# Kernel optimization log

Hardware: AMD Instinct MI355X
Metric: run time of the kernel (lower is better)

## Reference

```python
import jax, jax.numpy as jnp
import numpy as np

N_NODES = 10000
DIM = 512
HEADS = 8
HEAD_DIM = DIM // HEADS  # 64
TOPK = 6
EPS = 1e-5
SLOPE = 0.01  # torch LeakyReLU default


def _layernorm(x, w, b):
    mu = x.mean(axis=-1, keepdims=True)
    var = ((x - mu) ** 2).mean(axis=-1, keepdims=True)
    return (x - mu) / jnp.sqrt(var + EPS) * w + b


def setup_inputs() -> dict:
    key = jax.random.key(0)
    ks = jax.random.split(key, 8)

    def w(k, shape):
        return jax.random.normal(k, shape, dtype=jnp.float32) * 0.02

    return {
        "x": jax.random.normal(ks[0], (1, N_NODES, DIM), dtype=jnp.float32),
        "fc1_w": w(ks[1], (DIM, DIM)), "fc1_b": jnp.zeros((DIM,), jnp.float32),
        "wh_w": w(ks[2], (DIM, DIM)), "wh_b": jnp.zeros((DIM,), jnp.float32),
        "wt_w": w(ks[3], (DIM, DIM)), "wt_b": jnp.zeros((DIM,), jnp.float32),
        "q_w": w(ks[4], (DIM, DIM)), "q_b": jnp.zeros((DIM,), jnp.float32),
        "kv_w": w(ks[5], (2 * DIM, DIM)), "kv_b": jnp.zeros((2 * DIM,), jnp.float32),
        "lin_w": w(ks[6], (DIM, DIM)), "lin_b": jnp.zeros((DIM,), jnp.float32),
        "norm_w": jnp.ones((DIM,), jnp.float32),
        "norm_b": jnp.zeros((DIM,), jnp.float32),
    }


def reference(x, fc1_w, fc1_b, wh_w, wh_b, wt_w, wt_b, q_w, q_b,
              kv_w, kv_b, lin_w, lin_b, norm_w, norm_b):
    # x: [1, N, DIM]
    n = x.shape[1]
    scale = HEAD_DIM ** -0.5

    x_input = x
    h = jax.nn.leaky_relu(x @ fc1_w.T + fc1_b, SLOPE)
    h = (h + h.mean(axis=1, keepdims=True)) * 0.5

    e_h = h @ wh_w.T + wh_b            # [1, N, DIM]
    e_t = h @ wt_w.T + wt_b            # [1, N, DIM]

    # dense graph-construction scores + per-row top-k neighbors
    logits = (e_h * scale) @ jnp.swapaxes(e_t, -2, -1)   # [1, N, N]
    _, topk_idx = jax.lax.top_k(logits, TOPK)            # [1, N, TOPK]

    # prototype node = most frequent tail index (torch unique+counts+argsort, top=1)
    counts = jnp.bincount(topk_idx.reshape(-1), length=n)
    top_node = jnp.argmax(counts)

    ins_top = jnp.take(x_input, top_node[None], axis=1)  # [1, 1, DIM]
    q_feat = jnp.take(h, top_node[None], axis=1)[0, 0]   # [DIM]

    # gather k=TOPK neighbor tail embeddings per node
    nb = e_t[0][topk_idx[0]]                              # [N, TOPK, DIM]

    q_heads = (q_feat @ q_w.T + q_b).reshape(HEADS, HEAD_DIM) * scale
    kv = (nb @ kv_w.T + kv_b).reshape(n, TOPK, 2, HEADS, HEAD_DIM)
    k_, v_ = kv[:, :, 0], kv[:, :, 1]                     # [N, TOPK, H, HD]

    attn = jnp.einsum('hd,nehd->nhe', q_heads, k_)        # [N, H, TOPK]
    attn = jax.nn.softmax(attn, axis=-1)
    out = jnp.einsum('nhe,nehd->nhd', attn, v_).reshape(n, DIM)

    e_nh = _layernorm(out, norm_w, norm_b)[None]          # [1, N, DIM]

    s = _layernorm(e_h + e_nh, norm_w, norm_b)
    s = jax.nn.leaky_relu(s @ lin_w.T + lin_b, SLOPE)     # dropout = identity (eval)
    embedding = s + x_input
    return embedding, ins_top
```

## Files before the change

kernel.cpp:

```cpp
#include <hip/hip_runtime.h>
#include <hip/hip_bf16.h>
#include <math.h>

#define N_NODES 10000
#define DIM 512
#define TOPK 6
#define NCHUNK 10
#define CHUNK 1024
#define NL 4
#define NCK 8
#define NC2 16
#define SLOPE 0.01
#define LN_EPS 1e-5f
#define NB_COL 320

typedef short bf16x8 __attribute__((ext_vector_type(8)));
typedef float f32x4 __attribute__((ext_vector_type(4)));
typedef double f64x4 __attribute__((ext_vector_type(4)));

__device__ __forceinline__ unsigned pack_key(float v, int idx)
{
    unsigned b = __float_as_uint(v);
    unsigned m = b ^ ((unsigned)((int)b >> 31) | 0x80000000u);
    return (m & 0xFFFFC000u) | (16383u - (unsigned)idx);
}

template <int D>
__device__ __forceinline__ void insert_u(unsigned (&k)[D], unsigned nk)
{
    if (nk > k[D - 1]) {
        k[D - 1] = nk;
#pragma unroll
        for (int s = D - 1; s > 0; s--) {
            unsigned hi = max(k[s], k[s - 1]);
            unsigned lo = min(k[s], k[s - 1]);
            k[s - 1] = hi; k[s] = lo;
        }
    }
}

__device__ __forceinline__ void gload16(const void* g, void* l)
{
    __builtin_amdgcn_global_load_lds(
        (const __attribute__((address_space(1))) void*)g,
        (__attribute__((address_space(3))) void*)l, 16, 0, 0);
}

__global__ __launch_bounds__(256) void colsum_part64(
    const double* __restrict__ h, double* __restrict__ part, int n, int nb)
{
    int b = blockIdx.x;
    int rows_per = (n + nb - 1) / nb;
    int r0 = b * rows_per, r1 = min(n, r0 + rows_per);
    int t = threadIdx.x;
    double s0 = 0.0, s1 = 0.0;
    for (int i = r0; i < r1; i++) {
        s0 += h[(size_t)i * DIM + t];
        s1 += h[(size_t)i * DIM + t + 256];
    }
    part[b * DIM + t] = s0;
    part[b * DIM + t + 256] = s1;
}

__global__ void colmean64(const double* __restrict__ part, double* __restrict__ mean,
                          int nb, int n)
{
    int j = blockIdx.x * blockDim.x + threadIdx.x;
    if (j < DIM) {
        double s = 0.0;
        for (int b = 0; b < nb; b++) s += part[b * DIM + j];
        mean[j] = s / (double)n;
    }
}

__global__ void cast_wb(const float* __restrict__ in1, short* __restrict__ o1, int n1,
                        const float* __restrict__ in2, short* __restrict__ o2)
{
    int i = (blockIdx.x * blockDim.x + threadIdx.x) * 4;
    const float* in = (i < n1) ? in1 + i : in2 + (i - n1);
    short* o = (i < n1) ? o1 + i : o2 + (i - n1);
    float4 f = *(const float4*)in;
    __hip_bfloat16 b0 = __float2bfloat16(f.x), b1 = __float2bfloat16(f.y);
    __hip_bfloat16 b2 = __float2bfloat16(f.z), b3 = __float2bfloat16(f.w);
    *(short4*)o = make_short4(*(short*)&b0, *(short*)&b1, *(short*)&b2, *(short*)&b3);
}

__global__ __launch_bounds__(256, 4) void gemm_fc1(
    const float* __restrict__ X, const float* __restrict__ W,
    const float* __restrict__ bias, double* __restrict__ C, int n)
{
    const int K = DIM, M = DIM;
    const int id = blockIdx.x;
    const int c = id & 7, kk2 = id >> 3;
    const int y = kk2 & 3, mm = kk2 >> 2;
    const int bx = c + 8 * mm;
    if (bx >= (n + 63) / 64) return;

    __shared__ double As[64][18];
    __shared__ double Bs[128][18];
    const int t = threadIdx.x, lane = t & 63, wid = t >> 6;
    const int lx = lane & 15, q = lane >> 4;
    const int wr = (wid >> 1) * 32, wc = (wid & 1) * 64;
    const int i0 = bx * 64, j0 = y * 128;

    f64x4 acc[2][4];
#pragma unroll
    for (int a = 0; a < 2; a++)
#pragma unroll
        for (int b = 0; b < 4; b++) acc[a][b] = (f64x4)0.0;

    const int arow = t >> 2, askq = (t & 3) * 4;
    int gi = i0 + arow; if (gi >= n) gi = n - 1;
    const float* af32 = X + (size_t)gi * K + askq;
    const int brow = t >> 1, bskq = (t & 1) * 8;
    const float* wrow = W + (size_t)(j0 + brow) * K + bskq;

    float4 wv0 = *(const float4*)(wrow);
    float4 wv1 = *(const float4*)(wrow + 4);
    float4 av = *(const float4*)(af32);

    for (int k0 = 0; k0 < K; k0 += 16) {
        __syncthreads();
        As[arow][askq]     = (double)av.x; As[arow][askq + 1] = (double)av.y;
        As[arow][askq + 2] = (double)av.z; As[arow][askq + 3] = (double)av.w;
        Bs[brow][bskq]     = (double)wv0.x; Bs[brow][bskq + 1] = (double)wv0.y;
        Bs[brow][bskq + 2] = (double)wv0.z; Bs[brow][bskq + 3] = (double)wv0.w;
        Bs[brow][bskq + 4] = (double)wv1.x; Bs[brow][bskq + 5] = (double)wv1.y;
        Bs[brow][bskq + 6] = (double)wv1.z; Bs[brow][bskq + 7] = (double)wv1.w;
        if (k0 + 16 < K) {
            wv0 = *(const float4*)(wrow + k0 + 16);
            wv1 = *(const float4*)(wrow + k0 + 20);
            av  = *(const float4*)(af32 + k0 + 16);
        }
        __syncthreads();

#pragma unroll
        for (int ks = 0; ks < 4; ks++) {
            double a0 = As[wr + lx][ks * 4 + q];
            double a1 = As[wr + 16 + lx][ks * 4 + q];
#pragma unroll
            for (int cf = 0; cf < 4; cf++) {
                double b = Bs[wc + cf * 16 + lx][ks * 4 + q];
                acc[0][cf] = __builtin_amdgcn_mfma_f64_16x16x4f64(a0, b, acc[0][cf], 0, 0, 0);
                acc[1][cf] = __builtin_amdgcn_mfma_f64_16x16x4f64(a1, b, acc[1][cf], 0, 0, 0);
            }
        }
    }

#pragma unroll
    for (int rf = 0; rf < 2; rf++)
#pragma unroll
        for (int cf = 0; cf < 4; cf++)
#pragma unroll
            for (int reg = 0; reg < 4; reg++) {
                int gi2 = i0 + wr + rf * 16 + q * 4 + reg;
                int gj2 = j0 + wc + cf * 16 + lx;
                if (gi2 < n) {
                    double v = acc[rf][cf][reg] + (double)bias[gj2];
                    v = (v >= 0.0) ? v : v * SLOPE;
                    C[(size_t)gi2 * M + gj2] = v;
                }
            }
}

__global__ __launch_bounds__(256, 4) void gemm_ehet(
    const double* __restrict__ H, const float* __restrict__ whw,
    const float* __restrict__ whb, const float* __restrict__ wtw,
    const float* __restrict__ wtb, const double* __restrict__ mn,
    double* __restrict__ ehd, float* __restrict__ ehf, short* __restrict__ ehb2,
    double* __restrict__ etd, short* __restrict__ etb2, int n)
{
    const int K = DIM, M = DIM;
    const int id = blockIdx.x;
    const int c = id & 7, kk2 = id >> 3;
    const int y = kk2 & 7, mm = kk2 >> 3;
    const int bx = c + 8 * mm;
    if (bx >= (n + 63) / 64) return;
    const bool isH = (y < 4);
    const float* W    = isH ? whw : wtw;
    const float* bias = isH ? whb : wtb;
    double* C  = isH ? ehd : etd;
    short*  ob = isH ? ehb2 : etb2;

    __shared__ double As[64][18];
    __shared__ double Bs[128][18];
    const int t = threadIdx.x, lane = t & 63, wid = t >> 6;
    const int lx = lane & 15, q = lane >> 4;
    const int wr = (wid >> 1) * 32, wc = (wid & 1) * 64;
    const int i0 = bx * 64, j0 = (y & 3) * 128;

    f64x4 acc[2][4];
#pragma unroll
    for (int a = 0; a < 2; a++)
#pragma unroll
        for (int b = 0; b < 4; b++) acc[a][b] = (f64x4)0.0;

    const int arow = t >> 2, askq = (t & 3) * 4;
    int gi = i0 + arow; if (gi >= n) gi = n - 1;
    const double* af64 = H + (size_t)gi * K + askq;
    const int brow = t >> 1, bskq = (t & 1) * 8;
    const float* wrow = W + (size_t)(j0 + brow) * K + bskq;

    float4 wv0 = *(const float4*)(wrow);
    float4 wv1 = *(const float4*)(wrow + 4);
    double2 a0v = *(const double2*)(af64);
    double2 a1v = *(const double2*)(af64 + 2);

    for (int k0 = 0; k0 < K; k0 += 16) {
        __syncthreads();
        double2 mv0 = *(const double2*)(mn + k0 + askq);
        double2 mv1 = *(const double2*)(mn + k0 + askq + 2);
        As[arow][askq]     = (a0v.x + mv0.x) * 0.5; As[arow][askq + 1] = (a0v.y + mv0.y) * 0.5;
        As[arow][askq + 2] = (a1v.x + mv1.x) * 0.5; As[arow][askq + 3] = (a1v.y + mv1.y) * 0.5;
        Bs[brow][bskq]     = (double)wv0.x; Bs[brow][bskq + 1] = (double)wv0.y;
        Bs[brow][bskq + 2] = (double)wv0.z; Bs[brow][bskq + 3] = (double)wv0.w;
        Bs[brow][bskq + 4] = (double)wv1.x; Bs[brow][bskq + 5] = (double)wv1.y;
        Bs[brow][bskq + 6] = (double)wv1.z; Bs[brow][bskq + 7] = (double)wv1.w;
        if (k0 + 16 < K) {
            wv0 = *(const float4*)(wrow + k0 + 16);
            wv1 = *(const float4*)(wrow + k0 + 20);
            a0v = *(const double2*)(af64 + k0 + 16);
            a1v = *(const double2*)(af64 + k0 + 18);
        }
        __syncthreads();

#pragma unroll
        for (int ks = 0; ks < 4; ks++) {
            double a0 = As[wr + lx][ks * 4 + q];
            double a1 = As[wr + 16 + lx][ks * 4 + q];
#pragma unroll
            for (int cf = 0; cf < 4; cf++) {
                double b = Bs[wc + cf * 16 + lx][ks * 4 + q];
                acc[0][cf] = __builtin_amdgcn_mfma_f64_16x16x4f64(a0, b, acc[0][cf], 0, 0, 0);
                acc[1][cf] = __builtin_amdgcn_mfma_f64_16x16x4f64(a1, b, acc[1][cf], 0, 0, 0);
            }
        }
    }

#pragma unroll
    for (int rf = 0; rf < 2; rf++)
#pragma unroll
        for (int cf = 0; cf < 4; cf++)
#pragma unroll
            for (int reg = 0; reg < 4; reg++) {
                int gi2 = i0 + wr + rf * 16 + q * 4 + reg;
                int gj2 = j0 + wc + cf * 16 + lx;
                if (gi2 < n) {
                    double v = acc[rf][cf][reg] + (double)bias[gj2];
                    size_t idx = (size_t)gi2 * M + gj2;
                    C[idx] = v;
                    float f = (float)v;
                    if (isH) ehf[idx] = f;
                    __hip_bfloat16 bb = __float2bfloat16(f);
                    ob[idx] = *reinterpret_cast<short*>(&bb);
                }
            }
}

__global__ __launch_bounds__(256, 3) void logits_topk_mfma(
    const short* __restrict__ eh, const short* __restrict__ et,
    unsigned* __restrict__ pk, int n)
{
    __shared__ short As[2][4096];
    __shared__ short Bs[2][4096];
    const int t = threadIdx.x;
    const int lane = t & 63, wid = t >> 6;
    const int lx = lane & 15, q = lane >> 4;

    int id = blockIdx.x, bx, chunk;
    if (id < 632) { chunk = id & 7; bx = id >> 3; }
    else { int r = id - 632; chunk = 8 + (r & 1); bx = r >> 1; }
    const int i0 = bx * 128;
    const int wbase = wid * 32;

    const int jlo = chunk * CHUNK;
    const int jhi = min(n, jlo + CHUNK);
    const int nj = (jhi - jlo + 127) >> 7;
    const int np = nj * 16;

    const int sslot = (t & 3) ^ ((t >> 3) & 3);
    const short* aP[2];
    const short* bP[2];
#pragma unroll
    for (int is = 0; is < 2; is++) {
        int row = is * 64 + (t >> 2);
        int ra = i0 + row; if (ra >= n) ra = n - 1;
        aP[is] = eh + (size_t)ra * DIM + sslot * 8;
    }
    const int slotq = (q ^ ((lx >> 1) & 3)) * 8;
    const int aOff = (wbase + lx) * 32 + slotq;
    const int bOff = lx * 32 + slotq;

    unsigned keys[8][NL];
#pragma unroll
    for (int r = 0; r < 8; r++)
#pragma unroll
        for (int s = 0; s < NL; s++) keys[r][s] = 0u;

    f32x4 acc[2][8];
#pragma unroll
    for (int rf = 0; rf < 2; rf++)
#pragma unroll
        for (int cf = 0; cf < 8; cf++) acc[rf][cf] = (f32x4)0.f;

    auto STAGE = [&](int buf, int ph) {
        int kk = ph & 15;
        if (kk == 0) {
            int j0 = jlo + (ph >> 4) * 128;
#pragma unroll
            for (int is = 0; is < 2; is++) {
                int row = is * 64 + (t >> 2);
                int rb = j0 + row; if (rb >= n) rb = n - 1;
                bP[is] = et + (size_t)rb * DIM + sslot * 8;
            }
        }
        int ko = kk * 32;
#pragma unroll
        for (int is = 0; is < 2; is++) {
            gload16(aP[is] + ko, &As[buf][is * 2048 + wid * 512]);
            gload16(bP[is] + ko, &Bs[buf][is * 2048 + wid * 512]);
        }
    };

    STAGE(0, 0);
    for (int p = 0; p < np; ++p) {
        __builtin_amdgcn_sched_barrier(0);
        __builtin_amdgcn_s_barrier();
        __builtin_amdgcn_sched_barrier(0);
        if (p + 1 < np) {
            STAGE((p + 1) & 1, p + 1);
            asm volatile("s_waitcnt vmcnt(4)" ::: "memory");
        } else {
            asm volatile("s_waitcnt vmcnt(0)" ::: "memory");
        }
        __builtin_amdgcn_sched_barrier(0);
        __builtin_amdgcn_s_barrier();
        __builtin_amdgcn_sched_barrier(0);

        const short* Ab = As[p & 1];
        const short* Bb = Bs[p & 1];
        bf16x8 a0 = *(const bf16x8*)(Ab + aOff);
        bf16x8 a1 = *(const bf16x8*)(Ab + aOff + 512);
#pragma unroll
        for (int cf = 0; cf < 8; cf++) {
            bf16x8 bw = *(const bf16x8*)(Bb + bOff + cf * 512);
            acc[0][cf] = __builtin_amdgcn_mfma_f32_16x16x32_bf16(
                a0, bw, acc[0][cf], 0, 0, 0);
            acc[1][cf] = __builtin_amdgcn_mfma_f32_16x16x32_bf16(
                a1, bw, acc[1][cf], 0, 0, 0);
        }

        if ((p & 15) == 15) {
            int j0 = jlo + (p >> 4) * 128;
#pragma unroll
            for (int rf = 0; rf < 2; rf++)
#pragma unroll
                for (int cf = 0; cf < 8; cf++) {
                    int gj = j0 + cf * 16 + lx;
                    if (gj < n) {
#pragma unroll
                        for (int reg = 0; reg < 4; reg++)
                            insert_u<NL>(keys[rf * 4 + reg],
                                         pack_key(acc[rf][cf][reg], gj));
                    }
                    acc[rf][cf] = (f32x4)0.f;
                }
        }
    }

#pragma unroll
    for (int rr = 0; rr < 8; rr++) {
        unsigned mk[NCK];
#pragma unroll
        for (int s = 0; s < NL; s++) mk[s] = keys[rr][s];
#pragma unroll
        for (int s = NL; s < NCK; s++) mk[s] = 0u;
        for (int m = 1; m < 16; m <<= 1) {
            unsigned sv[NCK];
#pragma unroll
            for (int s = 0; s < NCK; s++) sv[s] = mk[s];
#pragma unroll
            for (int s = 0; s < NCK; s++) {
                unsigned ov = (unsigned)__shfl_xor((int)sv[s], m);
                insert_u<NCK>(mk, ov);
            }
        }
        if (lx == 0) {
            int rf = rr >> 2, reg = rr & 3;
            int grow = i0 + wbase + rf * 16 + q * 4 + reg;
            if (grow < n) {
#pragma unroll
                for (int s = 0; s < NCK; s++)
                    pk[((size_t)chunk * N_NODES + grow) * NCK + s] = mk[s];
            }
        }
    }
}

template <int POST, int NY, int LY>
__global__ __launch_bounds__(256, 3) void mfma_gemm_bf16(
    const short* __restrict__ A, const short* __restrict__ W,
    const float* __restrict__ bias, const float* __restrict__ res,
    float* __restrict__ C, int n, int M)
{
    const int id = blockIdx.x;
    const int c = id & 7, kk2 = id >> 3;
    const int y = kk2 & (NY - 1), mm = kk2 >> LY;
    const int bxx = c + 8 * mm;
    if (bxx >= (n + 127) / 128) return;

    __shared__ short As[2][8192];
    __shared__ short Bs[2][8192];
    const int t = threadIdx.x;
    const int lane = t & 63, wid = t >> 6;
    const int lx = lane & 15, q = lane >> 4;
    const int lx7 = lane & 7;
    const int i0 = bxx * 128;
    const int j0 = y * 128;
    const int wbase = wid * 32;
    const int srl = lane >> 3;
    const int swz = (lane & 7) ^ srl;

    const short* aP[4];
    const short* bP[4];
#pragma unroll
    for (int is = 0; is < 4; is++) {
        int ra = i0 + is * 32 + wid * 8 + srl; if (ra >= n) ra = n - 1;
        aP[is] = A + (size_t)ra * DIM + swz * 8;
        int rb = j0 + is * 32 + wid * 8 + srl;
        bP[is] = W + (size_t)rb * DIM + swz * 8;
    }
    int aIdx[2], bIdx[2];
#pragma unroll
    for (int ks = 0; ks < 2; ks++) {
        int kap = (ks * 4 + q) ^ lx7;
        aIdx[ks] = (wbase + lx) * 64 + kap * 8;
        bIdx[ks] = lx * 64 + kap * 8;
    }

    f32x4 acc[2][8];
#pragma unroll
    for (int rf = 0; rf < 2; rf++)
#pragma unroll
        for (int cf = 0; cf < 8; cf++) acc[rf][cf] = (f32x4)0.f;

    auto STAGE = [&](int buf, int kk) {
        int ko = kk * 64;
        short* ab = &As[buf][wid * 512];
        short* bb = &Bs[buf][wid * 512];
#pragma unroll
        for (int is = 0; is < 4; is++) {
            gload16(aP[is] + ko, ab + is * 2048);
            gload16(bP[is] + ko, bb + is * 2048);
        }
    };

    STAGE(0, 0);
    for (int p = 0; p < 8; ++p) {
        __builtin_amdgcn_sched_barrier(0);
        __builtin_amdgcn_s_barrier();
        __builtin_amdgcn_sched_barrier(0);
        if (p + 1 < 8) {
            STAGE((p + 1) & 1, p + 1);
            asm volatile("s_waitcnt vmcnt(8)" ::: "memory");
        } else {
            asm volatile("s_waitcnt vmcnt(0)" ::: "memory");
        }
        __builtin_amdgcn_sched_barrier(0);
        __builtin_amdgcn_s_barrier();
        __builtin_amdgcn_sched_barrier(0);

        const short* Ab = As[p & 1];
        const short* Bb = Bs[p & 1];
#pragma unroll
        for (int ks = 0; ks < 2; ks++) {
            bf16x8 a0 = *(const bf16x8*)(Ab + aIdx[ks]);
            bf16x8 a1 = *(const bf16x8*)(Ab + aIdx[ks] + 1024);
#pragma unroll
            for (int cf = 0; cf < 8; cf++) {
                bf16x8 bw = *(const bf16x8*)(Bb + bIdx[ks] + cf * 1024);
                acc[0][cf] = __builtin_amdgcn_mfma_f32_16x16x32_bf16(
                    a0, bw, acc[0][cf], 0, 0, 0);
                acc[1][cf] = __builtin_amdgcn_mfma_f32_16x16x32_bf16(
                    a1, bw, acc[1][cf], 0, 0, 0);
            }
        }
    }

#pragma unroll
    for (int rf = 0; rf < 2; rf++)
#pragma unroll
        for (int cf = 0; cf < 8; cf++)
#pragma unroll
            for (int reg = 0; reg < 4; reg++) {
                int gi = i0 + wbase + rf * 16 + q * 4 + reg;
                int gj = j0 + cf * 16 + lx;
                if (gi < n) {
                    float v = acc[rf][cf][reg] + bias[gj];
                    if (POST >= 1) v = (v >= 0.f) ? v : v * SLOPE;
                    if (POST == 2) v += res[(size_t)gi * M + gj];
                    C[(size_t)gi * M + gj] = v;
                }
            }
}

__global__ void merge_chunks16(const unsigned* __restrict__ pk,
                               int* __restrict__ cand, int n)
{
    int row = blockIdx.x * blockDim.x + threadIdx.x;
    if (row >= n) return;
    unsigned bk[NC2];
#pragma unroll
    for (int s = 0; s < NC2; s++) bk[s] = 0u;
    for (int c = 0; c < NCHUNK; c++) {
#pragma unroll
        for (int s = 0; s < NCK; s++)
            insert_u<NC2>(bk, pk[((size_t)c * n + row) * NCK + s]);
    }
#pragma unroll
    for (int s = 0; s < NC2; s++)
        cand[row * NC2 + s] = 16383 - (int)(bk[s] & 16383u);
}

__global__ __launch_bounds__(256) void refine16(
    const double* __restrict__ ehd, const double* __restrict__ etd,
    const int* __restrict__ cand, int* __restrict__ tki,
    int* __restrict__ counts, int n)
{
    int row = blockIdx.x * 4 + (threadIdx.x >> 6);
    if (row >= n) return;
    int lane = threadIdx.x & 63;
    int c = lane >> 2, sub = lane & 3;
    int j = cand[row * NC2 + c];
    const double* er = ehd + (size_t)row * DIM;
    const double* tr = etd + (size_t)j * DIM;
    double s = 0.0;
#pragma unroll 8
    for (int k = sub; k < DIM; k += 4) s += er[k] * tr[k];
    s += __shfl_down(s, 2);
    s += __shfl_down(s, 1);
    double mine = __shfl(s, lane & ~3);
    int rank = 0;
#pragma unroll
    for (int m = 0; m < NC2; m++) {
        double vm = __shfl(s, m * 4);
        int jm = __shfl(j, m * 4);
        bool better = (vm > mine) || (vm == mine && jm < j);
        rank += better ? 1 : 0;
    }
    if (sub == 0 && rank < TOPK) {
        tki[row * TOPK + rank] = j;
        atomicAdd(&counts[j], 1);
    }
}

__global__ __launch_bounds__(1024) void argmax_kernel(
    const int* __restrict__ counts, int n, const float* __restrict__ x,
    int* __restrict__ topn, float* __restrict__ out_ins)
{
    __shared__ unsigned long long red[1024];
    int t = threadIdx.x;
    unsigned long long best = 0;
    for (int j = t; j < n; j += 1024) {
        unsigned long long key =
            ((unsigned long long)(unsigned)counts[j] << 32) | (unsigned)(n - 1 - j);
        if (key > best) best = key;
    }
    red[t] = best;
    __syncthreads();
    for (int s = 512; s > 0; s >>= 1) {
        if (t < s && red[t + s] > red[t]) red[t] = red[t + s];
        __syncthreads();
    }
    int tn = n - 1 - (int)(red[0] & 0xffffffffu);
    if (t == 0) *topn = tn;
    if (t < DIM) out_ins[t] = x[(size_t)tn * DIM + t];
}

__global__ __launch_bounds__(512) void qheads_kernel(
    const double* __restrict__ h2d, const double* __restrict__ mn,
    const int* __restrict__ topn, const float* __restrict__ qw,
    const float* __restrict__ qb, float* __restrict__ qh)
{
    __shared__ float qf[DIM];
    int t = threadIdx.x;
    int tn = *topn;
    qf[t] = (float)((h2d[(size_t)tn * DIM + t] + mn[t]) * 0.5);
    __syncthreads();
    int w = t >> 6, lane = t & 63;
    int jrow = blockIdx.x * 8 + w;
    float s = 0.f;
    for (int k = lane; k < DIM; k += 64) s += qf[k] * qw[(size_t)jrow * DIM + k];
#pragma unroll
    for (int m = 32; m > 0; m >>= 1) s += __shfl_down(s, m);
    if (lane == 0) qh[jrow] = (s + qb[jrow]) * 0.125f;
}

__global__ __launch_bounds__(512) void scores_kernel(
    const float* __restrict__ E, const float* __restrict__ qh, float* __restrict__ sc)
{
    int i = blockIdx.x;
    int t = threadIdx.x, w = t >> 6, lane = t & 63;
    float v = qh[t] * E[(size_t)i * 1024 + t];
#pragma unroll
    for (int m = 32; m > 0; m >>= 1) v += __shfl_down(v, m);
    if (lane == 0) sc[i * 8 + w] = v;
}

__global__ __launch_bounds__(512) void attn_ln_kernel(
    const float* __restrict__ E, const float* __restrict__ sc,
    const int* __restrict__ tki, const float* __restrict__ eh,
    const float* __restrict__ nw, const float* __restrict__ nbias,
    short* __restrict__ sprb, int n)
{
    __shared__ int nb[TOPK];
    __shared__ float red[16];
    __shared__ float stats[2];
    const int i = blockIdx.x;
    const int t = threadIdx.x;
    const int h = t >> 6, lane = t & 63;
    if (t < TOPK) nb[t] = tki[i * TOPK + t];
    __syncthreads();

    float myse = 0.f;
    if (lane < TOPK) myse = sc[(size_t)nb[lane] * 8 + h];
    float se[TOPK];
#pragma unroll
    for (int e = 0; e < TOPK; e++) se[e] = __shfl(myse, e);
    float mx = se[0];
#pragma unroll
    for (int e = 1; e < TOPK; e++) mx = fmaxf(mx, se[e]);
    float wsum = 0.f, w[TOPK];
#pragma unroll
    for (int e = 0; e < TOPK; e++) { w[e] = expf(se[e] - mx); wsum += w[e]; }
    float inv = 1.f / wsum;

    float o = 0.f;
#pragma unroll
    for (int e = 0; e < TOPK; e++) o += w[e] * E[(size_t)nb[e] * 1024 + 512 + t];
    o *= inv;

    float s1 = o, s2 = o * o;
#pragma unroll
    for (int m = 32; m > 0; m >>= 1) { s1 += __shfl_down(s1, m); s2 += __shfl_down(s2, m); }
    if (lane == 0) { red[h] = s1; red[h + 8] = s2; }
    __syncthreads();
    if (t == 0) {
        float a = 0.f, b = 0.f;
#pragma unroll
        for (int k = 0; k < 8; k++) { a += red[k]; b += red[k + 8]; }
        float mu = a * (1.f / 512.f);
        float var = b * (1.f / 512.f) - mu * mu;
        stats[0] = mu; stats[1] = rsqrtf(var + LN_EPS);
    }
    __syncthreads();
    float enh = (o - stats[0]) * stats[1] * nw[t] + nbias[t];
    float t2 = eh[(size_t)i * DIM + t] + enh;
    __syncthreads();

    s1 = t2; s2 = t2 * t2;
#pragma unroll
    for (int m = 32; m > 0; m >>= 1) { s1 += __shfl_down(s1, m); s2 += __shfl_down(s2, m); }
    if (lane == 0) { red[h] = s1; red[h + 8] = s2; }
    __syncthreads();
    if (t == 0) {
        float a = 0.f, b = 0.f;
#pragma unroll
        for (int k = 0; k < 8; k++) { a += red[k]; b += red[k + 8]; }
        float mu = a * (1.f / 512.f);
        float var = b * (1.f / 512.f) - mu * mu;
        stats[0] = mu; stats[1] = rsqrtf(var + LN_EPS);
    }
    __syncthreads();
    float sv = (t2 - stats[0]) * stats[1] * nw[t] + nbias[t];
    __hip_bfloat16 bb = __float2bfloat16(sv);
    sprb[(size_t)i * DIM + t] = *reinterpret_cast<short*>(&bb);
}

extern "C" void kernel_launch(void* const* d_in, const int* in_sizes, int n_in,
                              void* d_out, int out_size, void* d_ws, size_t ws_size,
                              hipStream_t stream)
{
    const float* x     = (const float*)d_in[0];
    const float* fc1_w = (const float*)d_in[1];
    const float* fc1_b = (const float*)d_in[2];
    const float* wh_w  = (const float*)d_in[3];
    const float* wh_b  = (const float*)d_in[4];
    const float* wt_w  = (const float*)d_in[5];
    const float* wt_b  = (const float*)d_in[6];
    const float* q_w   = (const float*)d_in[7];
    const float* q_b   = (const float*)d_in[8];
    const float* kv_w  = (const float*)d_in[9];
    const float* kv_b  = (const float*)d_in[10];
    const float* lin_w = (const float*)d_in[11];
    const float* lin_b = (const float*)d_in[12];
    const float* nw    = (const float*)d_in[13];
    const float* nbias = (const float*)d_in[14];
    float* out = (float*)d_out;

    const int n = N_NODES;
    size_t off = 0;
    auto take = [&](size_t bytes) -> void* {
        void* p = (void*)((char*)d_ws + off);
        off += (bytes + 255) & ~(size_t)255;
        return p;
    };
    double* h2d  = (double*)take((size_t)n * DIM * 8);
    double* ehd  = (double*)take((size_t)n * DIM * 8);
    double* etd  = (double*)take((size_t)n * DIM * 8);
    float*  ehf  = (float*)take((size_t)n * DIM * 4);
    short*  ehb  = (short*)take((size_t)n * DIM * 2);
    short*  etb  = (short*)take((size_t)n * DIM * 2);
    short*  sprb = (short*)take((size_t)n * DIM * 2);
    unsigned* pk = (unsigned*)take((size_t)NCHUNK * n * NCK * 4);
    int*    cand = (int*)take((size_t)n * NC2 * 4);
    int*    tki  = (int*)take((size_t)n * TOPK * 4);
    int*    counts = (int*)take((size_t)n * 4);
    int*    topn = (int*)take(256);
    float*  qh   = (float*)take(DIM * 4);
    float*  sc   = (float*)take((size_t)n * 8 * 4);
    double* part = (double*)take((size_t)NB_COL * DIM * 8);
    double* mean = (double*)take(DIM * 8);
    short*  kvwb = (short*)take((size_t)1024 * DIM * 2);
    short*  linwb = (short*)take((size_t)512 * DIM * 2);
    float* E = (float*)h2d;

    hipMemsetAsync(counts, 0, n * sizeof(int), stream);

    dim3 b256(256);
    const int RB2 = (n + 127) / 128;

    gemm_fc1<<<dim3(640), b256, 0, stream>>>(x, fc1_w, fc1_b, h2d, n);
    colsum_part64<<<dim3(NB_COL), b256, 0, stream>>>(h2d, part, n, NB_COL);
    colmean64<<<dim3(2), b256, 0, stream>>>(part, mean, NB_COL, n);
    gemm_ehet<<<dim3(1280), b256, 0, stream>>>(
        h2d, wh_w, wh_b, wt_w, wt_b, mean, ehd, ehf, ehb, etd, etb, n);
    cast_wb<<<dim3((1536 * DIM) / 1024), b256, 0, stream>>>(
        kv_w, kvwb, 1024 * DIM, lin_w, linwb);

    logits_topk_mfma<<<dim3(632 + 2 * RB2), b256, 0, stream>>>(ehb, etb, pk, n);
    merge_chunks16<<<dim3((n + 255) / 256), b256, 0, stream>>>(pk, cand, n);
    refine16<<<dim3((n + 3) / 4), b256, 0, stream>>>(ehd, etd, cand, tki, counts, n);

    argmax_kernel<<<dim3(1), dim3(1024), 0, stream>>>(counts, n, x, topn,
                                                      out + (size_t)n * DIM);
    qheads_kernel<<<dim3(64), dim3(512), 0, stream>>>(h2d, mean, topn, q_w, q_b, qh);
    mfma_gemm_bf16<0, 8, 3><<<dim3(640), b256, 0, stream>>>(
        etb, kvwb, kv_b, nullptr, E, n, 1024);
    scores_kernel<<<dim3(n), dim3(512), 0, stream>>>(E, qh, sc);
    attn_ln_kernel<<<dim3(n), dim3(512), 0, stream>>>(E, sc, tki, ehf, nw, nbias, sprb, n);
    mfma_gemm_bf16<2, 4, 2><<<dim3(320), b256, 0, stream>>>(
        sprb, linwb, lin_b, x, out, n, 512);
}
```

Baseline: 829.3 us.

## Enlarge logits tile to 256 rows with half-size chunks; double K-step in f64 GEMMs

The logits/top-k kernel now gives each block 256 query rows (64 per wave) instead of 128, and splits the column range into 20 chunks of 512 instead of 10 of 1024. Each B tile is therefore reused across more MFMAs, and the grid stays near 800 blocks. The merge kernel now scans 20 partial candidate lists, which doubles the pk buffer traffic. The fp64 fc1 and eh/et GEMMs also move from a K step of 16 to 32 per shared-memory stage, which halves barrier count but costs more LDS and a lower launch-bounds occupancy target.

```diff
diff --git a/kernel.cpp b/kernel.cpp
--- a/kernel.cpp
+++ b/kernel.cpp
@@ -5,8 +5,8 @@
 #define N_NODES 10000
 #define DIM 512
 #define TOPK 6
-#define NCHUNK 10
-#define CHUNK 1024
+#define NHC 20
+#define HCHUNK 512
 #define NL 4
 #define NCK 8
 #define NC2 16
@@ -85,7 +85,7 @@
     *(short4*)o = make_short4(*(short*)&b0, *(short*)&b1, *(short*)&b2, *(short*)&b3);
 }
 
-__global__ __launch_bounds__(256, 4) void gemm_fc1(
+__global__ __launch_bounds__(256, 3) void gemm_fc1(
     const float* __restrict__ X, const float* __restrict__ W,
     const float* __restrict__ bias, double* __restrict__ C, int n)
 {
@@ -96,8 +96,8 @@
     const int bx = c + 8 * mm;
     if (bx >= (n + 63) / 64) return;
 
-    __shared__ double As[64][18];
-    __shared__ double Bs[128][18];
+    __shared__ double As[64][33];
+    __shared__ double Bs[128][33];
     const int t = threadIdx.x, lane = t & 63, wid = t >> 6;
     const int lx = lane & 15, q = lane >> 4;
     const int wr = (wid >> 1) * 32, wc = (wid & 1) * 64;
@@ -109,33 +109,45 @@
 #pragma unroll
         for (int b = 0; b < 4; b++) acc[a][b] = (f64x4)0.0;
 
-    const int arow = t >> 2, askq = (t & 3) * 4;
+    const int arow = t >> 2, askq = (t & 3) * 8;
     int gi = i0 + arow; if (gi >= n) gi = n - 1;
     const float* af32 = X + (size_t)gi * K + askq;
-    const int brow = t >> 1, bskq = (t & 1) * 8;
+    const int brow = t >> 1, bskq = (t & 1) * 16;
     const float* wrow = W + (size_t)(j0 + brow) * K + bskq;
 
     float4 wv0 = *(const float4*)(wrow);
     float4 wv1 = *(const float4*)(wrow + 4);
-    float4 av = *(const float4*)(af32);
-
-    for (int k0 = 0; k0 < K; k0 += 16) {
+    float4 wv2 = *(const float4*)(wrow + 8);
+    float4 wv3 = *(const float4*)(wrow + 12);
+    float4 av0 = *(const float4*)(af32);
+    float4 av1 = *(const float4*)(af32 + 4);
+
+    for (int k0 = 0; k0 < K; k0 += 32) {
         __syncthreads();
-        As[arow][askq]     = (double)av.x; As[arow][askq + 1] = (double)av.y;
-        As[arow][askq + 2] = (double)av.z; As[arow][askq + 3] = (double)av.w;
-        Bs[brow][bskq]     = (double)wv0.x; Bs[brow][bskq + 1] = (double)wv0.y;
-        Bs[brow][bskq + 2] = (double)wv0.z; Bs[brow][bskq + 3] = (double)wv0.w;
-        Bs[brow][bskq + 4] = (double)wv1.x; Bs[brow][bskq + 5] = (double)wv1.y;
-        Bs[brow][bskq + 6] = (double)wv1.z; Bs[brow][bskq + 7] = (double)wv1.w;
-        if (k0 + 16 < K) {
-            wv0 = *(const float4*)(wrow + k0 + 16);
-            wv1 = *(const float4*)(wrow + k0 + 20);
-            av  = *(const float4*)(af32 + k0 + 16);
+        As[arow][askq]     = (double)av0.x; As[arow][askq + 1] = (double)av0.y;
+        As[arow][askq + 2] = (double)av0.z; As[arow][askq + 3] = (double)av0.w;
+        As[arow][askq + 4] = (double)av1.x; As[arow][askq + 5] = (double)av1.y;
+        As[arow][askq + 6] = (double)av1.z; As[arow][askq + 7] = (double)av1.w;
+        Bs[brow][bskq]      = (double)wv0.x; Bs[brow][bskq + 1]  = (double)wv0.y;
+        Bs[brow][bskq + 2]  = (double)wv0.z; Bs[brow][bskq + 3]  = (double)wv0.w;
+        Bs[brow][bskq + 4]  = (double)wv1.x; Bs[brow][bskq + 5]  = (double)wv1.y;
+        Bs[brow][bskq + 6]  = (double)wv1.z; Bs[brow][bskq + 7]  = (double)wv1.w;
+        Bs[brow][bskq + 8]  = (double)wv2.x; Bs[brow][bskq + 9]  = (double)wv2.y;
+        Bs[brow][bskq + 10] = (double)wv2.z; Bs[brow][bskq + 11] = (double)wv2.w;
+        Bs[brow][bskq + 12] = (double)wv3.x; Bs[brow][bskq + 13] = (double)wv3.y;
+        Bs[brow][bskq + 14] = (double)wv3.z; Bs[brow][bskq + 15] = (double)wv3.w;
+        if (k0 + 32 < K) {
+            wv0 = *(const float4*)(wrow + k0 + 32);
+            wv1 = *(const float4*)(wrow + k0 + 36);
+            wv2 = *(const float4*)(wrow + k0 + 40);
+            wv3 = *(const float4*)(wrow + k0 + 44);
+            av0 = *(const float4*)(af32 + k0 + 32);
+            av1 = *(const float4*)(af32 + k0 + 36);
         }
         __syncthreads();
 
 #pragma unroll
-        for (int ks = 0; ks < 4; ks++) {
+        for (int ks = 0; ks < 8; ks++) {
             double a0 = As[wr + lx][ks * 4 + q];
             double a1 = As[wr + 16 + lx][ks * 4 + q];
 #pragma unroll
@@ -163,7 +175,7 @@
             }
 }
 
-__global__ __launch_bounds__(256, 4) void gemm_ehet(
+__global__ __launch_bounds__(256, 3) void gemm_ehet(
     const double* __restrict__ H, const float* __restrict__ whw,
     const float* __restrict__ whb, const float* __restrict__ wtw,
     const float* __restrict__ wtb, const double* __restrict__ mn,
@@ -182,8 +194,8 @@
     double* C  = isH ? ehd : etd;
     short*  ob = isH ? ehb2 : etb2;
 
-    __shared__ double As[64][18];
-    __shared__ double Bs[128][18];
+    __shared__ double As[64][33];
+    __shared__ double Bs[128][33];
     const int t = threadIdx.x, lane = t & 63, wid = t >> 6;
     const int lx = lane & 15, q = lane >> 4;
     const int wr = (wid >> 1) * 32, wc = (wid & 1) * 64;
@@ -195,37 +207,53 @@
 #pragma unroll
         for (int b = 0; b < 4; b++) acc[a][b] = (f64x4)0.0;
 
-    const int arow = t >> 2, askq = (t & 3) * 4;
+    const int arow = t >> 2, askq = (t & 3) * 8;
     int gi = i0 + arow; if (gi >= n) gi = n - 1;
     const double* af64 = H + (size_t)gi * K + askq;
-    const int brow = t >> 1, bskq = (t & 1) * 8;
+    const int brow = t >> 1, bskq = (t & 1) * 16;
     const float* wrow = W + (size_t)(j0 + brow) * K + bskq;
 
     float4 wv0 = *(const float4*)(wrow);
     float4 wv1 = *(const float4*)(wrow + 4);
+    float4 wv2 = *(const float4*)(wrow + 8);
+    float4 wv3 = *(const float4*)(wrow + 12);
     double2 a0v = *(const double2*)(af64);
     double2 a1v = *(const double2*)(af64 + 2);
-
-    for (int k0 = 0; k0 < K; k0 += 16) {
+    double2 a2v = *(const double2*)(af64 + 4);
+    double2 a3v = *(const double2*)(af64 + 6);
+
+    for (int k0 = 0; k0 < K; k0 += 32) {
         __syncthreads();
         double2 mv0 = *(const double2*)(mn + k0 + askq);
         double2 mv1 = *(const double2*)(mn + k0 + askq + 2);
+        double2 mv2 = *(const double2*)(mn + k0 + askq + 4);
+        double2 mv3 = *(const double2*)(mn + k0 + askq + 6);
         As[arow][askq]     = (a0v.x + mv0.x) * 0.5; As[arow][askq + 1] = (a0v.y + mv0.y) * 0.5;
         As[arow][askq + 2] = (a1v.x + mv1.x) * 0.5; As[arow][askq + 3] = (a1v.y + mv1.y) * 0.5;
-        Bs[brow][bskq]     = (double)wv0.x; Bs[brow][bskq + 1] = (double)wv0.y;
-        Bs[brow][bskq + 2] = (double)wv0.z; Bs[brow][bskq + 3] = (double)wv0.w;
-        Bs[brow][bskq + 4] = (double)wv1.x; Bs[brow][bskq + 5] = (double)wv1.y;
-        Bs[brow][bskq + 6] = (double)wv1.z; Bs[brow][bskq + 7] = (double)wv1.w;
-        if (k0 + 16 < K) {
-            wv0 = *(const float4*)(wrow + k0 + 16);
-            wv1 = *(const float4*)(wrow + k0 + 20);
-            a0v = *(const double2*)(af64 + k0 + 16);
-            a1v = *(const double2*)(af64 + k0 + 18);
+        As[arow][askq + 4] = (a2v.x + mv2.x) * 0.5; As[arow][askq + 5] = (a2v.y + mv2.y) * 0.5;
+        As[arow][askq + 6] = (a3v.x + mv3.x) * 0.5; As[arow][askq + 7] = (a3v.y + mv3.y) * 0.5;
+        Bs[brow][bskq]      = (double)wv0.x; Bs[brow][bskq + 1]  = (double)wv0.y;
+        Bs[brow][bskq + 2]  = (double)wv0.z; Bs[brow][bskq + 3]  = (double)wv0.w;
+        Bs[brow][bskq + 4]  = (double)wv1.x; Bs[brow][bskq + 5]  = (double)wv1.y;
+        Bs[brow][bskq + 6]  = (double)wv1.z; Bs[brow][bskq + 7]  = (double)wv1.w;
+        Bs[brow][bskq + 8]  = (double)wv2.x; Bs[brow][bskq + 9]  = (double)wv2.y;
+        Bs[brow][bskq + 10] = (double)wv2.z; Bs[brow][bskq + 11] = (double)wv2.w;
+        Bs[brow][bskq + 12] = (double)wv3.x; Bs[brow][bskq + 13] = (double)wv3.y;
+        Bs[brow][bskq + 14] = (double)wv3.z; Bs[brow][bskq + 15] = (double)wv3.w;
+        if (k0 + 32 < K) {
+            wv0 = *(const float4*)(wrow + k0 + 32);
+            wv1 = *(const float4*)(wrow + k0 + 36);
+            wv2 = *(const float4*)(wrow + k0 + 40);
+            wv3 = *(const float4*)(wrow + k0 + 44);
+            a0v = *(const double2*)(af64 + k0 + 32);
+            a1v = *(const double2*)(af64 + k0 + 34);
+            a2v = *(const double2*)(af64 + k0 + 36);
+            a3v = *(const double2*)(af64 + k0 + 38);
         }
         __syncthreads();
 
 #pragma unroll
-        for (int ks = 0; ks < 4; ks++) {
+        for (int ks = 0; ks < 8; ks++) {
             double a0 = As[wr + lx][ks * 4 + q];
             double a1 = As[wr + 16 + lx][ks * 4 + q];
 #pragma unroll
@@ -257,32 +285,32 @@
             }
 }
 
-__global__ __launch_bounds__(256, 3) void logits_topk_mfma(
+__global__ __launch_bounds__(256, 2) void logits_topk_mfma(
     const short* __restrict__ eh, const short* __restrict__ et,
     unsigned* __restrict__ pk, int n)
 {
-    __shared__ short As[2][4096];
+    __shared__ short As[2][8192];
     __shared__ short Bs[2][4096];
     const int t = threadIdx.x;
     const int lane = t & 63, wid = t >> 6;
     const int lx = lane & 15, q = lane >> 4;
 
-    int id = blockIdx.x, bx, chunk;
-    if (id < 632) { chunk = id & 7; bx = id >> 3; }
-    else { int r = id - 632; chunk = 8 + (r & 1); bx = r >> 1; }
-    const int i0 = bx * 128;
-    const int wbase = wid * 32;
-
-    const int jlo = chunk * CHUNK;
-    const int jhi = min(n, jlo + CHUNK);
+    int id = blockIdx.x, bx, hc;
+    if (id < 640) { hc = id & 15; bx = id >> 4; }
+    else { int r = id - 640; hc = 16 + (r & 3); bx = r >> 2; }
+    const int i0 = bx * 256;
+    const int wbase = wid * 64;
+
+    const int jlo = hc * HCHUNK;
+    const int jhi = min(n, jlo + HCHUNK);
     const int nj = (jhi - jlo + 127) >> 7;
     const int np = nj * 16;
 
     const int sslot = (t & 3) ^ ((t >> 3) & 3);
-    const short* aP[2];
+    const short* aP[4];
     const short* bP[2];
 #pragma unroll
-    for (int is = 0; is < 2; is++) {
+    for (int is = 0; is < 4; is++) {
         int row = is * 64 + (t >> 2);
         int ra = i0 + row; if (ra >= n) ra = n - 1;
         aP[is] = eh + (size_t)ra * DIM + sslot * 8;
@@ -291,15 +319,15 @@
     const int aOff = (wbase + lx) * 32 + slotq;
     const int bOff = lx * 32 + slotq;
 
-    unsigned keys[8][NL];
-#pragma unroll
-    for (int r = 0; r < 8; r++)
+    unsigned keys[16][NL];
+#pragma unroll
+    for (int r = 0; r < 16; r++)
 #pragma unroll
         for (int s = 0; s < NL; s++) keys[r][s] = 0u;
 
-    f32x4 acc[2][8];
-#pragma unroll
-    for (int rf = 0; rf < 2; rf++)
+    f32x4 acc[4][8];
+#pragma unroll
+    for (int rf = 0; rf < 4; rf++)
 #pragma unroll
         for (int cf = 0; cf < 8; cf++) acc[rf][cf] = (f32x4)0.f;
 
@@ -316,10 +344,11 @@
         }
         int ko = kk * 32;
 #pragma unroll
-        for (int is = 0; is < 2; is++) {
+        for (int is = 0; is < 4; is++)
             gload16(aP[is] + ko, &As[buf][is * 2048 + wid * 512]);
+#pragma unroll
+        for (int is = 0; is < 2; is++)
             gload16(bP[is] + ko, &Bs[buf][is * 2048 + wid * 512]);
-        }
     };
 
     STAGE(0, 0);
@@ -329,7 +358,7 @@
         __builtin_amdgcn_sched_barrier(0);
         if (p + 1 < np) {
             STAGE((p + 1) & 1, p + 1);
-            asm volatile("s_waitcnt vmcnt(4)" ::: "memory");
+            asm volatile("s_waitcnt vmcnt(6)" ::: "memory");
         } else {
             asm volatile("s_waitcnt vmcnt(0)" ::: "memory");
         }
@@ -341,19 +370,21 @@
         const short* Bb = Bs[p & 1];
         bf16x8 a0 = *(const bf16x8*)(Ab + aOff);
         bf16x8 a1 = *(const bf16x8*)(Ab + aOff + 512);
+        bf16x8 a2 = *(const bf16x8*)(Ab + aOff + 1024);
+        bf16x8 a3 = *(const bf16x8*)(Ab + aOff + 1536);
 #pragma unroll
         for (int cf = 0; cf < 8; cf++) {
             bf16x8 bw = *(const bf16x8*)(Bb + bOff + cf * 512);
-            acc[0][cf] = __builtin_amdgcn_mfma_f32_16x16x32_bf16(
-                a0, bw, acc[0][cf], 0, 0, 0);
-            acc[1][cf] = __builtin_amdgcn_mfma_f32_16x16x32_bf16(
-                a1, bw, acc[1][cf], 0, 0, 0);
+            acc[0][cf] = __builtin_amdgcn_mfma_f32_16x16x32_bf16(a0, bw, acc[0][cf], 0, 0, 0);
+            acc[1][cf] = __builtin_amdgcn_mfma_f32_16x16x32_bf16(a1, bw, acc[1][cf], 0, 0, 0);
+            acc[2][cf] = __builtin_amdgcn_mfma_f32_16x16x32_bf16(a2, bw, acc[2][cf], 0, 0, 0);
+            acc[3][cf] = __builtin_amdgcn_mfma_f32_16x16x32_bf16(a3, bw, acc[3][cf], 0, 0, 0);
         }
 
         if ((p & 15) == 15) {
             int j0 = jlo + (p >> 4) * 128;
 #pragma unroll
-            for (int rf = 0; rf < 2; rf++)
+            for (int rf = 0; rf < 4; rf++)
 #pragma unroll
                 for (int cf = 0; cf < 8; cf++) {
                     int gj = j0 + cf * 16 + lx;
@@ -369,7 +400,7 @@
     }
 
 #pragma unroll
-    for (int rr = 0; rr < 8; rr++) {
+    for (int rr = 0; rr < 16; rr++) {
         unsigned mk[NCK];
 #pragma unroll
         for (int s = 0; s < NL; s++) mk[s] = keys[rr][s];
@@ -391,7 +422,7 @@
             if (grow < n) {
 #pragma unroll
                 for (int s = 0; s < NCK; s++)
-                    pk[((size_t)chunk * N_NODES + grow) * NCK + s] = mk[s];
+                    pk[((size_t)hc * N_NODES + grow) * NCK + s] = mk[s];
             }
         }
     }
@@ -512,7 +543,7 @@
     unsigned bk[NC2];
 #pragma unroll
     for (int s = 0; s < NC2; s++) bk[s] = 0u;
-    for (int c = 0; c < NCHUNK; c++) {
+    for (int c = 0; c < NHC; c++) {
 #pragma unroll
         for (int s = 0; s < NCK; s++)
             insert_u<NC2>(bk, pk[((size_t)c * n + row) * NCK + s]);
@@ -712,7 +743,7 @@
     short*  ehb  = (short*)take((size_t)n * DIM * 2);
     short*  etb  = (short*)take((size_t)n * DIM * 2);
     short*  sprb = (short*)take((size_t)n * DIM * 2);
-    unsigned* pk = (unsigned*)take((size_t)NCHUNK * n * NCK * 4);
+    unsigned* pk = (unsigned*)take((size_t)NHC * n * NCK * 4);
     int*    cand = (int*)take((size_t)n * NC2 * 4);
     int*    tki  = (int*)take((size_t)n * TOPK * 4);
     int*    counts = (int*)take((size_t)n * 4);
@@ -728,7 +759,6 @@
     hipMemsetAsync(counts, 0, n * sizeof(int), stream);
 
     dim3 b256(256);
-    const int RB2 = (n + 127) / 128;
 
     gemm_fc1<<<dim3(640), b256, 0, stream>>>(x, fc1_w, fc1_b, h2d, n);
     colsum_part64<<<dim3(NB_COL), b256, 0, stream>>>(h2d, part, n, NB_COL);
@@ -738,7 +768,7 @@
     cast_wb<<<dim3((1536 * DIM) / 1024), b256, 0, stream>>>(
         kv_w, kvwb, 1024 * DIM, lin_w, linwb);
 
-    logits_topk_mfma<<<dim3(632 + 2 * RB2), b256, 0, stream>>>(ehb, etb, pk, n);
+    logits_topk_mfma<<<dim3(800), b256, 0, stream>>>(ehb, etb, pk, n);
     merge_chunks16<<<dim3((n + 255) / 256), b256, 0, stream>>>(pk, cand, n);
     refine16<<<dim3((n + 3) / 4), b256, 0, stream>>>(ehd, etd, cand, tki, counts, n);
 
```

Result: slower. 909.1 us (+9.6%).
